# Performance work log

Measured on AMD Instinct MI355X. Metric: run time of the kernel, lower is better.

## Reference

```python
import jax, jax.numpy as jnp
import numpy as np

IN_SIZE, Q_SIZE, V_SIZE = 1024, 128, 1024
B, S = 8, 2048


def setup_inputs() -> dict:
    key = jax.random.key(0)
    ks = jax.random.split(key, 7)
    scale = 1.0 / np.sqrt(IN_SIZE)
    x = jax.random.normal(ks[0], (B, S, IN_SIZE), dtype=jnp.float32)
    Wq = jax.random.uniform(ks[1], (IN_SIZE, Q_SIZE), dtype=jnp.float32, minval=-scale, maxval=scale)
    bq = jax.random.uniform(ks[2], (Q_SIZE,), dtype=jnp.float32, minval=-scale, maxval=scale)
    Wk = jax.random.uniform(ks[3], (IN_SIZE, Q_SIZE), dtype=jnp.float32, minval=-scale, maxval=scale)
    bk = jax.random.uniform(ks[4], (Q_SIZE,), dtype=jnp.float32, minval=-scale, maxval=scale)
    Wv = jax.random.uniform(ks[5], (IN_SIZE, V_SIZE), dtype=jnp.float32, minval=-scale, maxval=scale)
    bv = jax.random.uniform(ks[6], (V_SIZE,), dtype=jnp.float32, minval=-scale, maxval=scale)
    return {"x": x, "Wq": Wq, "bq": bq, "Wk": Wk, "bk": bk, "Wv": Wv, "bv": bv}


def reference(x, Wq, bq, Wk, bk, Wv, bv):
    # Projections: [B, S, q_size] / [B, S, v_size]
    q = jnp.einsum('bsi,iq->bsq', x, Wq) + bq
    k = jnp.einsum('bsi,iq->bsq', x, Wk) + bk
    v = jnp.einsum('bsi,iv->bsv', x, Wv) + bv
    # Unscaled attention scores [B, S, S] (module has no 1/sqrt(d) scale)
    scores = jnp.einsum('bsq,btq->bst', q, k)
    attn = jax.nn.softmax(scores, axis=-1)
    out = jnp.einsum('bst,btv->bsv', attn, v)
    return jnp.tanh(out)
```

## Files before the change

kernel.cpp:

```cpp
#include <hip/hip_runtime.h>
#include <hip/hip_bf16.h>
#include <stdint.h>

#define BM 128
#define BN 128
#define BK 64

typedef __attribute__((ext_vector_type(8))) short    bf16x8;
typedef __attribute__((ext_vector_type(8))) _Float16 f16x8;
typedef __attribute__((ext_vector_type(4))) float    f32x4;

typedef __attribute__((address_space(1))) void GV;
typedef __attribute__((address_space(3))) void LV;

__device__ __forceinline__ unsigned short f2bf(float f){
  union { float f; unsigned u; } x; x.f = f;
  unsigned r = x.u + 0x7fffu + ((x.u >> 16) & 1u);
  return (unsigned short)(r >> 16);
}
__device__ __forceinline__ float bf2f(unsigned short h){
  union { unsigned u; float f; } x; x.u = ((unsigned)h) << 16; return x.f;
}
__device__ __forceinline__ unsigned short f2h(float f){
  union { _Float16 h; unsigned short u; } c; c.h = (_Float16)f; return c.u;
}

template<bool F16>
__device__ __forceinline__ void mma16(f32x4& acc, bf16x8 a, bf16x8 b){
  if constexpr (F16)
    acc = __builtin_amdgcn_mfma_f32_16x16x32_f16(__builtin_bit_cast(f16x8, a),
                                                 __builtin_bit_cast(f16x8, b), acc, 0, 0, 0);
  else
    acc = __builtin_amdgcn_mfma_f32_16x16x32_bf16(a, b, acc, 0, 0, 0);
}

#define SBAR() { __builtin_amdgcn_sched_barrier(0); __builtin_amdgcn_s_barrier(); __builtin_amdgcn_sched_barrier(0); }
#define LGKM0() { asm volatile("s_waitcnt lgkmcnt(0)" ::: "memory"); __builtin_amdgcn_sched_barrier(0); }

__device__ __forceinline__ bf16x8 frag_ld(const unsigned short* lds, int r, int k){
  int byte = ((r << 7) + (k << 1)) ^ ((r & 7) << 4);
  return *(const bf16x8*)((const char*)lds + byte);
}

__device__ __forceinline__ void stage_tile(const unsigned short* __restrict__ src, int ld,
                                           unsigned short* lds, int tid){
  #pragma unroll
  for (int t = 0; t < 4; ++t){
    int idx = t*256 + tid;
    int row = idx >> 3;
    int kc  = (idx & 7) ^ (row & 7);
    const unsigned short* g = src + (size_t)row*ld + kc*8;
    __builtin_amdgcn_global_load_lds((GV*)g, (LV*)(lds + idx*8), 16, 0, 0);
  }
}

template<bool F16>
__device__ __forceinline__ void gemm_core(const unsigned short* __restrict__ At,
                                          const unsigned short* __restrict__ Bt,
                                          int lda, int ldb, int nkt,
                                          unsigned short* lsA, unsigned short* lsB,
                                          f32x4 (&acc)[4][4]){
  const int tid  = threadIdx.x;
  const int lane = tid & 63;
  const int wr = ((tid >> 7) & 1) << 6;
  const int wc = ((tid >> 6) & 1) << 6;
  const int l15 = lane & 15, lg = lane >> 4;

  for (int kt = 0; kt < nkt; ++kt){
    stage_tile(At + (size_t)kt*BK, lda, lsA, tid);
    stage_tile(Bt + (size_t)kt*BK, ldb, lsB, tid);
    __syncthreads();
    #pragma unroll
    for (int kk = 0; kk < 2; ++kk){
      bf16x8 af[4], bfr[4];
      #pragma unroll
      for (int mf = 0; mf < 4; ++mf) af[mf]  = frag_ld(lsA, wr + mf*16 + l15, kk*32 + lg*8);
      #pragma unroll
      for (int nf = 0; nf < 4; ++nf) bfr[nf] = frag_ld(lsB, wc + nf*16 + l15, kk*32 + lg*8);
      #pragma unroll
      for (int mf = 0; mf < 4; ++mf)
        #pragma unroll
        for (int nf = 0; nf < 4; ++nf)
          mma16<F16>(acc[mf][nf], af[mf], bfr[nf]);
    }
    __syncthreads();
  }
}

#define ZERO_ACC4(acc) { _Pragma("unroll") for (int i_=0;i_<4;++i_) _Pragma("unroll") for (int j_=0;j_<4;++j_) acc[i_][j_] = (f32x4){0.f,0.f,0.f,0.f}; }


__device__ __forceinline__ void stg2(const unsigned short* g, size_t qq, unsigned short* d){
  __builtin_amdgcn_global_load_lds((GV*)g, (LV*)d, 16, 0, 0);
  __builtin_amdgcn_global_load_lds((GV*)(g + qq), (LV*)(d + 4096), 16, 0, 0);
}

template<bool F16, int BUF>
__device__ __forceinline__ void ktile256(int t, int nkt,
    const unsigned short*& gA0, const unsigned short*& gA1,
    const unsigned short*& gB0, const unsigned short*& gB1,
    size_t qA, size_t qB,
    unsigned short* dA, unsigned short* dB,
    const char* lA_k0, const char* lA_k1, const char* lB_k0, const char* lB_k1,
    f32x4 (&acc)[8][4]){
  bf16x8 af[4], bfr[4];

  #pragma unroll
  for (int i = 0; i < 4; ++i) af[i]  = *(const bf16x8*)(lA_k0 + BUF*32768 + i*2048);
  #pragma unroll
  for (int i = 0; i < 4; ++i) bfr[i] = *(const bf16x8*)(lB_k0 + BUF*32768 + i*2048);
  if (t + 1 < nkt) stg2(gA0 + 64, qA, dA + (BUF^1)*16384);
  SBAR(); LGKM0();
  __builtin_amdgcn_s_setprio(1);
  #pragma unroll
  for (int mf = 0; mf < 4; ++mf)
    #pragma unroll
    for (int nf = 0; nf < 4; ++nf) mma16<F16>(acc[mf][nf], af[mf], bfr[nf]);
  __builtin_amdgcn_s_setprio(0);
  SBAR();

  #pragma unroll
  for (int i = 0; i < 4; ++i) af[i] = *(const bf16x8*)(lA_k0 + BUF*32768 + (4+i)*2048);
  if (t + 1 < nkt) stg2(gA1 + 64, qA, dA + (BUF^1)*16384 + 8192);
  SBAR(); LGKM0();
  __builtin_amdgcn_s_setprio(1);
  #pragma unroll
  for (int mf = 0; mf < 4; ++mf)
    #pragma unroll
    for (int nf = 0; nf < 4; ++nf) mma16<F16>(acc[mf+4][nf], af[mf], bfr[nf]);
  __builtin_amdgcn_s_setprio(0);
  SBAR();

  #pragma unroll
  for (int i = 0; i < 4; ++i) af[i]  = *(const bf16x8*)(lA_k1 + BUF*32768 + i*2048);
  #pragma unroll
  for (int i = 0; i < 4; ++i) bfr[i] = *(const bf16x8*)(lB_k1 + BUF*32768 + i*2048);
  SBAR(); LGKM0();
  __builtin_amdgcn_s_setprio(1);
  #pragma unroll
  for (int mf = 0; mf < 4; ++mf)
    #pragma unroll
    for (int nf = 0; nf < 4; ++nf) mma16<F16>(acc[mf][nf], af[mf], bfr[nf]);
  __builtin_amdgcn_s_setprio(0);
  SBAR();

  #pragma unroll
  for (int i = 0; i < 4; ++i) af[i] = *(const bf16x8*)(lA_k1 + BUF*32768 + (4+i)*2048);
  if (t + 2 < nkt){
    stg2(gB0 + 128, qB, dB + BUF*16384);
    stg2(gB1 + 128, qB, dB + BUF*16384 + 8192);
    asm volatile("s_waitcnt vmcnt(4)" ::: "memory");
    __builtin_amdgcn_sched_barrier(0);
  } else if (t + 1 < nkt){
    asm volatile("s_waitcnt vmcnt(0)" ::: "memory");
    __builtin_amdgcn_sched_barrier(0);
  }
  SBAR(); LGKM0();
  __builtin_amdgcn_s_setprio(1);
  #pragma unroll
  for (int mf = 0; mf < 4; ++mf)
    #pragma unroll
    for (int nf = 0; nf < 4; ++nf) mma16<F16>(acc[mf+4][nf], af[mf], bfr[nf]);
  __builtin_amdgcn_s_setprio(0);
  SBAR();

  gA0 += 64; gA1 += 64; gB0 += 64; gB1 += 64;
}

template<bool F16>
__device__ __forceinline__ void gemm256(const unsigned short* __restrict__ Ab, int lda,
                                        const unsigned short* __restrict__ Bb, int ldb,
                                        int nkt, unsigned short* sm, f32x4 (&acc)[8][4]){
  const int tid  = threadIdx.x;
  const int lane = tid & 63, l15 = lane & 15, lg = lane >> 4;
  const int wid  = tid >> 6;
  const int wrow0 = (wid >> 2) << 7;
  const int wcol0 = (wid & 3) << 6;

  const int srow = tid >> 3;
  const int scol = ((tid & 7) ^ (srow & 7)) << 3;
  const unsigned short* gA0 = Ab + (size_t)srow*lda + scol;
  const unsigned short* gA1 = gA0 + (size_t)128*lda;
  const unsigned short* gB0 = Bb + (size_t)srow*ldb + scol;
  const unsigned short* gB1 = gB0 + (size_t)128*ldb;
  const size_t qA = (size_t)64*lda, qB = (size_t)64*ldb;
  unsigned short* dA = sm + tid*8;
  unsigned short* dB = sm + 32768 + tid*8;

  const int mswz = (l15 & 7) << 4;
  const char* smc = (const char*)sm;
  const char* lA_k0 = smc + ((wrow0 + l15) << 7) + (((lg << 4))      ^ mswz);
  const char* lA_k1 = smc + ((wrow0 + l15) << 7) + ((64 + (lg << 4)) ^ mswz);
  const char* lB_k0 = smc + 65536 + ((wcol0 + l15) << 7) + (((lg << 4))      ^ mswz);
  const char* lB_k1 = smc + 65536 + ((wcol0 + l15) << 7) + ((64 + (lg << 4)) ^ mswz);

  stg2(gA0, qA, dA);          stg2(gA1, qA, dA + 8192);
  stg2(gB0, qB, dB);          stg2(gB1, qB, dB + 8192);
  stg2(gB0 + 64, qB, dB + 16384);
  stg2(gB1 + 64, qB, dB + 16384 + 8192);
  asm volatile("s_waitcnt vmcnt(4)" ::: "memory");
  __builtin_amdgcn_sched_barrier(0);
  SBAR();

  for (int t = 0; t < nkt; t += 2){
    ktile256<F16,0>(t,   nkt, gA0,gA1,gB0,gB1,qA,qB,dA,dB,lA_k0,lA_k1,lB_k0,lB_k1,acc);
    ktile256<F16,1>(t+1, nkt, gA0,gA1,gB0,gB1,qA,qB,dA,dB,lA_k0,lA_k1,lB_k0,lB_k1,acc);
  }
}

#define ZERO_ACC8(acc) { _Pragma("unroll") for (int i_=0;i_<8;++i_) _Pragma("unroll") for (int j_=0;j_<4;++j_) acc[i_][j_] = (f32x4){0.f,0.f,0.f,0.f}; }

__global__ __launch_bounds__(256) void k_cvt_x(const float* __restrict__ x,
                                               unsigned short* __restrict__ xh, int n4){
  int i = blockIdx.x*blockDim.x + threadIdx.x;
  int stride = gridDim.x*blockDim.x;
  for (; i < n4; i += stride){
    float4 v = ((const float4*)x)[i];
    ushort4 o; o.x = f2h(v.x); o.y = f2h(v.y); o.z = f2h(v.z); o.w = f2h(v.w);
    ((ushort4*)xh)[i] = o;
  }
}

__global__ __launch_bounds__(256) void k_cvt_wt(const float* __restrict__ Wq, const float* __restrict__ Wk,
                                                const float* __restrict__ Wv, unsigned short* __restrict__ Wt){
  int n = blockIdx.x*32 + threadIdx.x;
  int k = blockIdx.y*8  + threadIdx.y;
  float v;
  if (n < 128)      v = Wq[(size_t)k*128  + n];
  else if (n < 256) v = Wk[(size_t)k*128  + (n-128)];
  else              v = Wv[(size_t)k*1024 + (n-256)];
  Wt[(size_t)n*1024 + k] = f2h(v);
}

__global__ __launch_bounds__(256) void k_projQK(const unsigned short* __restrict__ xh,
                                                const unsigned short* __restrict__ Wt,
                                                const float* __restrict__ bq, const float* __restrict__ bk,
                                                unsigned short* __restrict__ Qh, unsigned short* __restrict__ Kh){
  __shared__ unsigned short lsA[BM*BK], lsB[BN*BK];
  const int m0  = blockIdx.x * BM;
  const int sel = blockIdx.y;
  f32x4 acc[4][4]; ZERO_ACC4(acc);
  gemm_core<true>(xh + (size_t)m0*1024, Wt + (size_t)sel*128*1024, 1024, 1024, 16, lsA, lsB, acc);

  const int tid = threadIdx.x, lane = tid & 63;
  const int wr = ((tid >> 7) & 1) << 6;
  const int wc = ((tid >> 6) & 1) << 6;
  const int l15 = lane & 15, lg = lane >> 4;

  unsigned short* T  = sel ? Kh : Qh;
  const float* bias  = sel ? bk : bq;
  #pragma unroll
  for (int mf = 0; mf < 4; ++mf){
    #pragma unroll
    for (int nf = 0; nf < 4; ++nf){
      int c = wc + nf*16 + l15;
      float bi = bias[c];
      #pragma unroll
      for (int r = 0; r < 4; ++r){
        int gr = m0 + wr + mf*16 + lg*4 + r;
        T[(size_t)gr*128 + c] = f2h(acc[mf][nf][r] + bi);
      }
    }
  }
}

__global__ __launch_bounds__(512, 2) void k_projV(const unsigned short* __restrict__ xh,
                                                  const unsigned short* __restrict__ Wt,
                                                  const float* __restrict__ bv,
                                                  unsigned short* __restrict__ Vt){
  extern __shared__ unsigned short sm[];
  const int bid = blockIdx.x;
  const int m0 = (bid & 63) << 8;
  const int n0 = (bid >> 6) << 8;

  f32x4 acc[8][4]; ZERO_ACC8(acc);
  gemm256<true>(xh + (size_t)m0*1024, 1024,
                Wt + (size_t)(256 + n0)*1024, 1024, 16, sm, acc);

  const int tid = threadIdx.x, lane = tid & 63, l15 = lane & 15, lg = lane >> 4;
  const int wid = tid >> 6;
  const int wrow0 = (wid >> 2) << 7;
  const int wcol0 = (wid & 3) << 6;

  #pragma unroll
  for (int mf = 0; mf < 8; ++mf){
    int gr0 = m0 + wrow0 + mf*16 + lg*4;
    int b = gr0 >> 11, t0 = gr0 & 2047;
    #pragma unroll
    for (int nf = 0; nf < 4; ++nf){
      int j = n0 + wcol0 + nf*16 + l15;
      float bi = bv[j];
      ushort4 pk;
      pk.x = f2bf(acc[mf][nf][0] + bi);
      pk.y = f2bf(acc[mf][nf][1] + bi);
      pk.z = f2bf(acc[mf][nf][2] + bi);
      pk.w = f2bf(acc[mf][nf][3] + bi);
      *(ushort4*)(Vt + ((size_t)b*1024 + j)*2048 + t0) = pk;
    }
  }
}

__global__ __launch_bounds__(256) void k_scores(const unsigned short* __restrict__ Qh,
                                                const unsigned short* __restrict__ Kh,
                                                unsigned short* __restrict__ P, float* __restrict__ lsum){
  __shared__ unsigned short lsA[BM*BK], lsB[BN*BK];
  const int s0 = blockIdx.x * BM;
  const int t0 = blockIdx.y * BN;
  const int b  = blockIdx.z;
  f32x4 acc[4][4]; ZERO_ACC4(acc);
  gemm_core<true>(Qh + ((size_t)b*2048 + s0)*128, Kh + ((size_t)b*2048 + t0)*128, 128, 128, 2, lsA, lsB, acc);

  unsigned short* Pb = P + (size_t)b*2048*2048;
  float* lb = lsum + b*2048;
  const int tid = threadIdx.x, lane = tid & 63;
  const int wr = ((tid >> 7) & 1) << 6;
  const int wc = ((tid >> 6) & 1) << 6;
  const int l15 = lane & 15, lg = lane >> 4;

  #pragma unroll
  for (int mf = 0; mf < 4; ++mf){
    #pragma unroll
    for (int r = 0; r < 4; ++r){
      int sr = s0 + wr + mf*16 + lg*4 + r;
      float rsum = 0.f;
      #pragma unroll
      for (int nf = 0; nf < 4; ++nf){
        float e = __expf(acc[mf][nf][r]);
        unsigned short h = f2bf(e);
        int tc = t0 + wc + nf*16 + l15;
        Pb[(size_t)sr*2048 + tc] = h;
        rsum += bf2f(h);
      }
      #pragma unroll
      for (int d = 1; d < 16; d <<= 1) rsum += __shfl_xor(rsum, d);
      if (l15 == 0) atomicAdd(&lb[sr], rsum);
    }
  }
}

__global__ __launch_bounds__(512, 2) void k_pv8(const unsigned short* __restrict__ P,
                                                const unsigned short* __restrict__ Vt,
                                                const float* __restrict__ lsum,
                                                float* __restrict__ out){
  extern __shared__ unsigned short sm[];
  const int bid = blockIdx.x;
  const int b   = bid & 7;
  const int r2  = bid >> 3;
  const int s0  = (r2 >> 2) << 8;
  const int j0  = (r2 & 3) << 8;

  f32x4 acc[8][4]; ZERO_ACC8(acc);
  gemm256<false>(P  + ((size_t)b*2048 + s0)*2048, 2048,
                 Vt + ((size_t)b*1024 + j0)*2048, 2048, 32, sm, acc);

  const int tid = threadIdx.x, lane = tid & 63, l15 = lane & 15, lg = lane >> 4;
  const int wid = tid >> 6;
  const int wrow0 = (wid >> 2) << 7;
  const int wcol0 = (wid & 3) << 6;

  const float* lb = lsum + b*2048;
  float* ob = out + (size_t)b*2048*1024;
  #pragma unroll
  for (int mf = 0; mf < 8; ++mf){
    #pragma unroll
    for (int r = 0; r < 4; ++r){
      int sr = s0 + wrow0 + mf*16 + lg*4 + r;
      float rl = 1.0f / lb[sr];
      #pragma unroll
      for (int nf = 0; nf < 4; ++nf){
        int jc = j0 + wcol0 + nf*16 + l15;
        float v = acc[mf][nf][r] * rl;
        ob[(size_t)sr*1024 + jc] = 1.0f - 2.0f/(1.0f + __expf(2.0f*v));
      }
    }
  }
}

extern "C" void kernel_launch(void* const* d_in, const int* in_sizes, int n_in,
                              void* d_out, int out_size, void* d_ws, size_t ws_size,
                              hipStream_t stream){
  const float* x  = (const float*)d_in[0];
  const float* Wq = (const float*)d_in[1];
  const float* bq = (const float*)d_in[2];
  const float* Wk = (const float*)d_in[3];
  const float* bk = (const float*)d_in[4];
  const float* Wv = (const float*)d_in[5];
  const float* bv = (const float*)d_in[6];
  float* out = (float*)d_out;

  char* ws = (char*)d_ws;
  const size_t MB = 1024*1024;
  unsigned short* Wt   = (unsigned short*)(ws);
  unsigned short* Qh   = (unsigned short*)(ws + 4*MB);
  unsigned short* Kh   = (unsigned short*)(ws + 8*MB);
  unsigned short* Vt   = (unsigned short*)(ws + 12*MB);
  unsigned short* P    = (unsigned short*)(ws + 44*MB);
  float*          lsum = (float*)(ws + 108*MB);
  unsigned short* xh   = (unsigned short*)d_out;

  hipMemsetAsync(lsum, 0, 16384*sizeof(float), stream);
  k_cvt_x  <<<2048, 256, 0, stream>>>(x, xh, 16384*1024/4);
  k_cvt_wt <<<dim3(40,128), dim3(32,8), 0, stream>>>(Wq, Wk, Wv, Wt);
  k_projQK <<<dim3(128,2), 256, 0, stream>>>(xh, Wt, bq, bk, Qh, Kh);
  k_projV  <<<256, 512, 131072, stream>>>(xh, Wt, bv, Vt);
  k_scores <<<dim3(16,16,8), 256, 0, stream>>>(Qh, Kh, P, lsum);
  k_pv8    <<<256, 512, 131072, stream>>>(P, Vt, lsum, out);
}
```

Measured before the change: 200.9 us.

## Software-pipeline LDS fragment loads across MFMA phases with double-buffered registers

Restructures the 256x256 GEMM k-tile loop so LDS fragment reads for the next MFMA phase are issued before the current phase's MFMAs, using ping-pong register fragments (afA/afB, bfrA/bfrB) and partial lgkmcnt waits instead of full waits. It also drops several barriers and reorders when global-to-LDS prefetches are issued and waited on. The aim is to hide LDS latency behind matrix-core work, at the cost of more live registers and subtler synchronization that could race on LDS buffer reuse.

```diff
diff --git a/kernel.cpp b/kernel.cpp
--- a/kernel.cpp
+++ b/kernel.cpp
@@ -35,7 +35,8 @@
 }
 
 #define SBAR() { __builtin_amdgcn_sched_barrier(0); __builtin_amdgcn_s_barrier(); __builtin_amdgcn_sched_barrier(0); }
-#define LGKM0() { asm volatile("s_waitcnt lgkmcnt(0)" ::: "memory"); __builtin_amdgcn_sched_barrier(0); }
+#define LGKM(n) { asm volatile("s_waitcnt lgkmcnt(" #n ")" ::: "memory"); __builtin_amdgcn_sched_barrier(0); }
+#define VMC(n)  { asm volatile("s_waitcnt vmcnt(" #n ")"  ::: "memory"); __builtin_amdgcn_sched_barrier(0); }
 
 __device__ __forceinline__ bf16x8 frag_ld(const unsigned short* lds, int r, int k){
   int byte = ((r << 7) + (k << 1)) ^ ((r & 7) << 4);
@@ -96,81 +97,83 @@
 }
 
 template<bool F16, int BUF>
-__device__ __forceinline__ void ktile256(int t, int nkt,
+__device__ __forceinline__ void ktile_pipe(int t, int nkt,
     const unsigned short*& gA0, const unsigned short*& gA1,
     const unsigned short*& gB0, const unsigned short*& gB1,
     size_t qA, size_t qB,
     unsigned short* dA, unsigned short* dB,
     const char* lA_k0, const char* lA_k1, const char* lB_k0, const char* lB_k1,
+    bf16x8 (&afA)[4], bf16x8 (&afB)[4], bf16x8 (&bfrA)[4], bf16x8 (&bfrB)[4],
     f32x4 (&acc)[8][4]){
-  bf16x8 af[4], bfr[4];
-
-  #pragma unroll
-  for (int i = 0; i < 4; ++i) af[i]  = *(const bf16x8*)(lA_k0 + BUF*32768 + i*2048);
-  #pragma unroll
-  for (int i = 0; i < 4; ++i) bfr[i] = *(const bf16x8*)(lB_k0 + BUF*32768 + i*2048);
-  if (t + 1 < nkt) stg2(gA0 + 64, qA, dA + (BUF^1)*16384);
-  SBAR(); LGKM0();
+
+  #pragma unroll
+  for (int i = 0; i < 4; ++i) afB[i] = *(const bf16x8*)(lA_k0 + BUF*32768 + (4+i)*2048);
+  if (t + 1 < nkt){
+    stg2(gA0 + 64, qA, dA + (BUF^1)*16384);
+    stg2(gA1 + 64, qA, dA + (BUF^1)*16384 + 8192);
+  }
+  LGKM(4);
   __builtin_amdgcn_s_setprio(1);
   #pragma unroll
   for (int mf = 0; mf < 4; ++mf)
     #pragma unroll
-    for (int nf = 0; nf < 4; ++nf) mma16<F16>(acc[mf][nf], af[mf], bfr[nf]);
+    for (int nf = 0; nf < 4; ++nf) mma16<F16>(acc[mf][nf], afA[mf], bfrA[nf]);
   __builtin_amdgcn_s_setprio(0);
   SBAR();
 
   #pragma unroll
-  for (int i = 0; i < 4; ++i) af[i] = *(const bf16x8*)(lA_k0 + BUF*32768 + (4+i)*2048);
-  if (t + 1 < nkt) stg2(gA1 + 64, qA, dA + (BUF^1)*16384 + 8192);
-  SBAR(); LGKM0();
+  for (int i = 0; i < 4; ++i) afA[i]  = *(const bf16x8*)(lA_k1 + BUF*32768 + i*2048);
+  #pragma unroll
+  for (int i = 0; i < 4; ++i) bfrB[i] = *(const bf16x8*)(lB_k1 + BUF*32768 + i*2048);
+  LGKM(8);
   __builtin_amdgcn_s_setprio(1);
   #pragma unroll
   for (int mf = 0; mf < 4; ++mf)
     #pragma unroll
-    for (int nf = 0; nf < 4; ++nf) mma16<F16>(acc[mf+4][nf], af[mf], bfr[nf]);
+    for (int nf = 0; nf < 4; ++nf) mma16<F16>(acc[mf+4][nf], afB[mf], bfrA[nf]);
   __builtin_amdgcn_s_setprio(0);
   SBAR();
 
   #pragma unroll
-  for (int i = 0; i < 4; ++i) af[i]  = *(const bf16x8*)(lA_k1 + BUF*32768 + i*2048);
-  #pragma unroll
-  for (int i = 0; i < 4; ++i) bfr[i] = *(const bf16x8*)(lB_k1 + BUF*32768 + i*2048);
-  SBAR(); LGKM0();
+  for (int i = 0; i < 4; ++i) afB[i] = *(const bf16x8*)(lA_k1 + BUF*32768 + (4+i)*2048);
+  LGKM(4);
   __builtin_amdgcn_s_setprio(1);
   #pragma unroll
   for (int mf = 0; mf < 4; ++mf)
     #pragma unroll
-    for (int nf = 0; nf < 4; ++nf) mma16<F16>(acc[mf][nf], af[mf], bfr[nf]);
+    for (int nf = 0; nf < 4; ++nf) mma16<F16>(acc[mf][nf], afA[mf], bfrB[nf]);
+  __builtin_amdgcn_s_setprio(0);
+  VMC(0);
+  SBAR();
+
+  if (t + 1 < nkt){
+    #pragma unroll
+    for (int i = 0; i < 4; ++i) afA[i]  = *(const bf16x8*)(lA_k0 + (BUF^1)*32768 + i*2048);
+    #pragma unroll
+    for (int i = 0; i < 4; ++i) bfrA[i] = *(const bf16x8*)(lB_k0 + (BUF^1)*32768 + i*2048);
+    if (t + 2 < nkt){
+      stg2(gB0 + 128, qB, dB + BUF*16384);
+      stg2(gB1 + 128, qB, dB + BUF*16384 + 8192);
+    }
+    LGKM(8);
+  } else {
+    LGKM(0);
+  }
+  __builtin_amdgcn_s_setprio(1);
+  #pragma unroll
+  for (int mf = 0; mf < 4; ++mf)
+    #pragma unroll
+    for (int nf = 0; nf < 4; ++nf) mma16<F16>(acc[mf+4][nf], afB[mf], bfrB[nf]);
   __builtin_amdgcn_s_setprio(0);
   SBAR();
 
-  #pragma unroll
-  for (int i = 0; i < 4; ++i) af[i] = *(const bf16x8*)(lA_k1 + BUF*32768 + (4+i)*2048);
-  if (t + 2 < nkt){
-    stg2(gB0 + 128, qB, dB + BUF*16384);
-    stg2(gB1 + 128, qB, dB + BUF*16384 + 8192);
-    asm volatile("s_waitcnt vmcnt(4)" ::: "memory");
-    __builtin_amdgcn_sched_barrier(0);
-  } else if (t + 1 < nkt){
-    asm volatile("s_waitcnt vmcnt(0)" ::: "memory");
-    __builtin_amdgcn_sched_barrier(0);
-  }
-  SBAR(); LGKM0();
-  __builtin_amdgcn_s_setprio(1);
-  #pragma unroll
-  for (int mf = 0; mf < 4; ++mf)
-    #pragma unroll
-    for (int nf = 0; nf < 4; ++nf) mma16<F16>(acc[mf+4][nf], af[mf], bfr[nf]);
-  __builtin_amdgcn_s_setprio(0);
-  SBAR();
-
   gA0 += 64; gA1 += 64; gB0 += 64; gB1 += 64;
 }
 
 template<bool F16>
-__device__ __forceinline__ void gemm256(const unsigned short* __restrict__ Ab, int lda,
-                                        const unsigned short* __restrict__ Bb, int ldb,
-                                        int nkt, unsigned short* sm, f32x4 (&acc)[8][4]){
+__device__ __forceinline__ void gemm256p(const unsigned short* __restrict__ Ab, int lda,
+                                         const unsigned short* __restrict__ Bb, int ldb,
+                                         int nkt, unsigned short* sm, f32x4 (&acc)[8][4]){
   const int tid  = threadIdx.x;
   const int lane = tid & 63, l15 = lane & 15, lg = lane >> 4;
   const int wid  = tid >> 6;
@@ -194,17 +197,24 @@
   const char* lB_k0 = smc + 65536 + ((wcol0 + l15) << 7) + (((lg << 4))      ^ mswz);
   const char* lB_k1 = smc + 65536 + ((wcol0 + l15) << 7) + ((64 + (lg << 4)) ^ mswz);
 
+  bf16x8 afA[4], afB[4], bfrA[4], bfrB[4];
+
   stg2(gA0, qA, dA);          stg2(gA1, qA, dA + 8192);
   stg2(gB0, qB, dB);          stg2(gB1, qB, dB + 8192);
   stg2(gB0 + 64, qB, dB + 16384);
   stg2(gB1 + 64, qB, dB + 16384 + 8192);
-  asm volatile("s_waitcnt vmcnt(4)" ::: "memory");
-  __builtin_amdgcn_sched_barrier(0);
+  VMC(4);
   SBAR();
+  #pragma unroll
+  for (int i = 0; i < 4; ++i) afA[i]  = *(const bf16x8*)(lA_k0 + i*2048);
+  #pragma unroll
+  for (int i = 0; i < 4; ++i) bfrA[i] = *(const bf16x8*)(lB_k0 + i*2048);
 
   for (int t = 0; t < nkt; t += 2){
-    ktile256<F16,0>(t,   nkt, gA0,gA1,gB0,gB1,qA,qB,dA,dB,lA_k0,lA_k1,lB_k0,lB_k1,acc);
-    ktile256<F16,1>(t+1, nkt, gA0,gA1,gB0,gB1,qA,qB,dA,dB,lA_k0,lA_k1,lB_k0,lB_k1,acc);
+    ktile_pipe<F16,0>(t,   nkt, gA0,gA1,gB0,gB1,qA,qB,dA,dB,
+                      lA_k0,lA_k1,lB_k0,lB_k1, afA,afB,bfrA,bfrB, acc);
+    ktile_pipe<F16,1>(t+1, nkt, gA0,gA1,gB0,gB1,qA,qB,dA,dB,
+                      lA_k0,lA_k1,lB_k0,lB_k1, afA,afB,bfrA,bfrB, acc);
   }
 }
 
@@ -274,8 +284,8 @@
   const int n0 = (bid >> 6) << 8;
 
   f32x4 acc[8][4]; ZERO_ACC8(acc);
-  gemm256<true>(xh + (size_t)m0*1024, 1024,
-                Wt + (size_t)(256 + n0)*1024, 1024, 16, sm, acc);
+  gemm256p<true>(xh + (size_t)m0*1024, 1024,
+                 Wt + (size_t)(256 + n0)*1024, 1024, 16, sm, acc);
 
   const int tid = threadIdx.x, lane = tid & 63, l15 = lane & 15, lg = lane >> 4;
   const int wid = tid >> 6;
@@ -350,8 +360,8 @@
   const int j0  = (r2 & 3) << 8;
 
   f32x4 acc[8][4]; ZERO_ACC8(acc);
-  gemm256<false>(P  + ((size_t)b*2048 + s0)*2048, 2048,
-                 Vt + ((size_t)b*1024 + j0)*2048, 2048, 32, sm, acc);
+  gemm256p<false>(P  + ((size_t)b*2048 + s0)*2048, 2048,
+                  Vt + ((size_t)b*1024 + j0)*2048, 2048, 32, sm, acc);
 
   const int tid = threadIdx.x, lane = tid & 63, l15 = lane & 15, lg = lane >> 4;
   const int wid = tid >> 6;
```

Result: slower. 233.3 us (+16.1%).
